# Performance work log

Hardware: AMD Instinct MI355X
Metric: run time of the kernel (lower is better)

## Reference

```python
import jax, jax.numpy as jnp
import numpy as np

D_MODEL = 1024
NUM_HEADS = 16
D_K = D_MODEL // NUM_HEADS


def setup_inputs() -> dict:
    key = jax.random.key(0)
    ks = jax.random.split(key, 11)
    B, S, D = 2, 2048, D_MODEL
    scale = 1.0 / np.sqrt(D)
    inp = {
        'queries': jax.random.normal(ks[0], (B, S, D), jnp.float32),
        'keys': jax.random.normal(ks[1], (B, S, D), jnp.float32),
        'values': jax.random.normal(ks[2], (B, S, D), jnp.float32),
        'w_q': jax.random.normal(ks[3], (D, D), jnp.float32) * scale,
        'b_q': jnp.zeros((D,), jnp.float32),
        'w_k': jax.random.normal(ks[4], (D, D), jnp.float32) * scale,
        'b_k': jnp.zeros((D,), jnp.float32),
        'w_v': jax.random.normal(ks[5], (D, D), jnp.float32) * scale,
        'b_v': jnp.zeros((D,), jnp.float32),
        'w_o': jax.random.normal(ks[6], (D, D), jnp.float32) * scale,
        'b_o': jnp.zeros((D,), jnp.float32),
    }
    return inp


def _split_heads(x):
    # [B, S, D] -> [B, H, S, d_k]
    B, S, _ = x.shape
    return x.reshape(B, S, NUM_HEADS, D_K).transpose(0, 2, 1, 3)


def reference(queries, keys, values, w_q, b_q, w_k, b_k, w_v, b_v, w_o, b_o):
    q = _split_heads(queries @ w_q.T + b_q)
    k = _split_heads(keys @ w_k.T + b_k)
    v = _split_heads(values @ w_v.T + b_v)
    # scaled dot-product attention: [B, H, Sq, Sk]
    scores = jnp.einsum('bhqd,bhkd->bhqk', q, k) / jnp.sqrt(jnp.asarray(D_K, q.dtype))
    weights = jax.nn.softmax(scores, axis=-1)
    attn = jnp.einsum('bhqk,bhkd->bhqd', weights, v)
    # merge heads: [B, Sq, D]
    B, H, S, dk = attn.shape
    merged = attn.transpose(0, 2, 1, 3).reshape(B, S, H * dk)
    return merged @ w_o.T + b_o
```

## Files before the change

kernel.cpp:

```cpp
#include <hip/hip_runtime.h>

typedef __attribute__((ext_vector_type(8))) short bf16x8;
typedef __attribute__((ext_vector_type(4))) short short4v;
typedef __attribute__((ext_vector_type(2))) unsigned int uint2v;
typedef __attribute__((ext_vector_type(4))) float f32x4;
typedef __attribute__((ext_vector_type(16))) float f32x16;
typedef __attribute__((ext_vector_type(4))) float float4v;
typedef unsigned short ushort_t;

__device__ __forceinline__ unsigned short f2bf(float x) {
    unsigned u = __float_as_uint(x);
    return (unsigned short)((u + 0x7fffu + ((u >> 16) & 1u)) >> 16);
}
__device__ __forceinline__ f32x4 mfma16(bf16x8 a, bf16x8 b, f32x4 c) {
    return __builtin_amdgcn_mfma_f32_16x16x32_bf16(a, b, c, 0, 0, 0);
}
__device__ __forceinline__ f32x16 mfma32(bf16x8 a, bf16x8 b, f32x16 c) {
    return __builtin_amdgcn_mfma_f32_32x32x16_bf16(a, b, c, 0, 0, 0);
}
__device__ __forceinline__ unsigned cvtpk(float lo, float hi) {
    unsigned r;
    asm("v_cvt_pk_bf16_f32 %0, %1, %2" : "=v"(r) : "v"(lo), "v"(hi));
    return r;
}
__device__ __forceinline__ bf16x8 pack4(unsigned w0, unsigned w1, unsigned w2, unsigned w3) {
    union { unsigned u[4]; bf16x8 v; } c;
    c.u[0] = w0; c.u[1] = w1; c.u[2] = w2; c.u[3] = w3;
    return c.v;
}

constexpr int GK = 1024;
constexpr int SLD = 72;
constexpr float QSCALE = 0.18033688011112042f;

__global__ __launch_bounds__(256)
void gemm_qkv2(const float* __restrict__ Aq, const float* __restrict__ Bq,
               const float* __restrict__ bq, ushort_t* __restrict__ Oq,
               const float* __restrict__ Ak, const float* __restrict__ Bk,
               const float* __restrict__ bk, ushort_t* __restrict__ Ok,
               const float* __restrict__ Avp, const float* __restrict__ Bv,
               const float* __restrict__ bv, ushort_t* __restrict__ Ov)
{
    __shared__ alignas(16) short Ah[128 * SLD];
    __shared__ alignas(16) short Bh[128 * SLD];

    const int bid = blockIdx.x;
    const int tid = threadIdx.x, lane = tid & 63, wv = tid >> 6;
    const int lr = lane & 15, lg = lane >> 4;
    const int r16 = tid >> 4, c4 = (tid & 15) * 4;

    if (bid < 512) {
        const int z = bid >> 8, fc = bid & 255;
        const float* A = z ? Ak : Aq;
        const float* B = z ? Bk : Bq;
        const float* bias = z ? bk : bq;
        ushort_t* O = z ? Ok : Oq;

        const int t = (fc & 7) * 32 + (fc >> 3);
        const int m0 = (t >> 3) * 128, n0 = (t & 7) * 128;
        const int wm = (wv >> 1) * 64, wn = (wv & 1) * 64;

        f32x4 acc[4][4] = {};
        float4v pfa[8], pfb[8];

        auto load_tiles = [&](int k0) {
            #pragma unroll
            for (int i = 0; i < 8; ++i) {
                pfa[i] = *(const float4v*)(A + (size_t)(m0 + r16 + 16 * i) * GK + k0 + c4);
                pfb[i] = *(const float4v*)(B + (size_t)(n0 + r16 + 16 * i) * GK + k0 + c4);
            }
        };
        auto store_tiles = [&]() {
            #pragma unroll
            for (int i = 0; i < 8; ++i) {
                uint2v wa, wb;
                wa.x = cvtpk(pfa[i][0], pfa[i][1]); wa.y = cvtpk(pfa[i][2], pfa[i][3]);
                wb.x = cvtpk(pfb[i][0], pfb[i][1]); wb.y = cvtpk(pfb[i][2], pfb[i][3]);
                *(uint2v*)(Ah + (r16 + 16 * i) * SLD + c4) = wa;
                *(uint2v*)(Bh + (r16 + 16 * i) * SLD + c4) = wb;
            }
        };

        load_tiles(0);
        for (int k0 = 0; k0 < GK; k0 += 64) {
            __syncthreads();
            store_tiles();
            __syncthreads();
            if (k0 + 64 < GK) load_tiles(k0 + 64);
            #pragma unroll
            for (int ks = 0; ks < 2; ++ks) {
                bf16x8 af[4], bfr[4];
                #pragma unroll
                for (int mi = 0; mi < 4; ++mi)
                    af[mi] = *(const bf16x8*)(Ah + (wm + mi * 16 + lr) * SLD + ks * 32 + lg * 8);
                #pragma unroll
                for (int ni = 0; ni < 4; ++ni)
                    bfr[ni] = *(const bf16x8*)(Bh + (wn + ni * 16 + lr) * SLD + ks * 32 + lg * 8);
                #pragma unroll
                for (int mi = 0; mi < 4; ++mi)
                    #pragma unroll
                    for (int ni = 0; ni < 4; ++ni)
                        acc[mi][ni] = mfma16(af[mi], bfr[ni], acc[mi][ni]);
            }
        }

        #pragma unroll
        for (int mi = 0; mi < 4; ++mi)
            #pragma unroll
            for (int ni = 0; ni < 4; ++ni) {
                const int gr = m0 + wm + mi * 16 + lg * 4;
                const int gc = n0 + wn + ni * 16 + lr;
                #pragma unroll
                for (int r = 0; r < 4; ++r) {
                    float val = acc[mi][ni][r] + bias[gc];
                    if (z == 0) val *= QSCALE;
                    O[(size_t)(gr + r) * 1024 + gc] = f2bf(val);
                }
            }
    } else {
        const int fc = bid - 512;
        const int t = (fc & 7) * 64 + (fc >> 3);
        const int nt = t >> 3, mt = t & 7;
        const int m0 = mt * 128, n0 = nt * 64;
        const int wm = (wv >> 1) * 64, wn = (wv & 1) * 32;

        f32x4 acc[4][2] = {};
        float4v pfa[8], pfb[4];

        auto load_tiles = [&](int k0) {
            #pragma unroll
            for (int i = 0; i < 8; ++i)
                pfa[i] = *(const float4v*)(Avp + (size_t)(m0 + r16 + 16 * i) * GK + k0 + c4);
            #pragma unroll
            for (int i = 0; i < 4; ++i)
                pfb[i] = *(const float4v*)(Bv + (size_t)(n0 + r16 + 16 * i) * GK + k0 + c4);
        };
        auto store_tiles = [&]() {
            #pragma unroll
            for (int i = 0; i < 8; ++i) {
                uint2v w;
                w.x = cvtpk(pfa[i][0], pfa[i][1]);
                w.y = cvtpk(pfa[i][2], pfa[i][3]);
                *(uint2v*)(Ah + (r16 + 16 * i) * SLD + c4) = w;
            }
            #pragma unroll
            for (int i = 0; i < 4; ++i) {
                uint2v w;
                w.x = cvtpk(pfb[i][0], pfb[i][1]);
                w.y = cvtpk(pfb[i][2], pfb[i][3]);
                *(uint2v*)(Bh + (r16 + 16 * i) * SLD + c4) = w;
            }
        };

        load_tiles(0);
        for (int k0 = 0; k0 < GK; k0 += 64) {
            __syncthreads();
            store_tiles();
            __syncthreads();
            if (k0 + 64 < GK) load_tiles(k0 + 64);
            #pragma unroll
            for (int ks = 0; ks < 2; ++ks) {
                bf16x8 af[4], bfr[2];
                #pragma unroll
                for (int mi = 0; mi < 4; ++mi)
                    af[mi] = *(const bf16x8*)(Ah + (wm + mi * 16 + lr) * SLD + ks * 32 + lg * 8);
                #pragma unroll
                for (int ni = 0; ni < 2; ++ni)
                    bfr[ni] = *(const bf16x8*)(Bh + (wn + ni * 16 + lr) * SLD + ks * 32 + lg * 8);
                #pragma unroll
                for (int mi = 0; mi < 4; ++mi)
                    #pragma unroll
                    for (int ni = 0; ni < 2; ++ni)
                        acc[mi][ni] = mfma16(af[mi], bfr[ni], acc[mi][ni]);
            }
        }

        #pragma unroll
        for (int mi = 0; mi < 4; ++mi)
            #pragma unroll
            for (int ni = 0; ni < 2; ++ni) {
                const int gr = m0 + wm + mi * 16 + lg * 4;
                const int gc = n0 + wn + ni * 16 + lr;
                #pragma unroll
                for (int r = 0; r < 4; ++r) {
                    float val = acc[mi][ni][r] + bv[gr + r];
                    Ov[(size_t)(gr + r) * 4096 + gc] = f2bf(val);
                }
            }
    }
}

__global__ __launch_bounds__(256)
void gemm_o(const ushort_t* __restrict__ A, const float* __restrict__ B,
            const float* __restrict__ bias, float* __restrict__ O)
{
    __shared__ alignas(16) short Ah[128 * SLD];
    __shared__ alignas(16) short Bh[64 * SLD];

    const int tid = threadIdx.x, lane = tid & 63, wv = tid >> 6;
    const int lr = lane & 15, lg = lane >> 4;

    const int f = blockIdx.x;
    const int t = (f & 7) * 64 + (f >> 3);
    const int mt = t >> 4, nt = t & 15;
    const int m0 = mt * 128, n0 = nt * 64;

    const int wm = (wv >> 1) * 64, wn = (wv & 1) * 32;
    const int r16 = tid >> 4, c4 = (tid & 15) * 4;
    const int r8 = tid >> 3, c8 = (tid & 7) * 8;

    f32x4 acc[4][2] = {};
    float4v pfb[4];
    bf16x8 pba[4];

    auto load_tiles = [&](int k0) {
        #pragma unroll
        for (int i = 0; i < 4; ++i)
            pba[i] = *(const bf16x8*)(A + (size_t)(m0 + r8 + 32 * i) * GK + k0 + c8);
        #pragma unroll
        for (int i = 0; i < 4; ++i)
            pfb[i] = *(const float4v*)(B + (size_t)(n0 + r16 + 16 * i) * GK + k0 + c4);
    };
    auto store_tiles = [&]() {
        #pragma unroll
        for (int i = 0; i < 4; ++i)
            *(bf16x8*)(Ah + (r8 + 32 * i) * SLD + c8) = pba[i];
        #pragma unroll
        for (int i = 0; i < 4; ++i) {
            uint2v w;
            w.x = cvtpk(pfb[i][0], pfb[i][1]);
            w.y = cvtpk(pfb[i][2], pfb[i][3]);
            *(uint2v*)(Bh + (r16 + 16 * i) * SLD + c4) = w;
        }
    };

    load_tiles(0);
    for (int k0 = 0; k0 < GK; k0 += 64) {
        __syncthreads();
        store_tiles();
        __syncthreads();
        if (k0 + 64 < GK) load_tiles(k0 + 64);
        #pragma unroll
        for (int ks = 0; ks < 2; ++ks) {
            bf16x8 af[4], bfr[2];
            #pragma unroll
            for (int mi = 0; mi < 4; ++mi)
                af[mi] = *(const bf16x8*)(Ah + (wm + mi * 16 + lr) * SLD + ks * 32 + lg * 8);
            #pragma unroll
            for (int ni = 0; ni < 2; ++ni)
                bfr[ni] = *(const bf16x8*)(Bh + (wn + ni * 16 + lr) * SLD + ks * 32 + lg * 8);
            #pragma unroll
            for (int mi = 0; mi < 4; ++mi)
                #pragma unroll
                for (int ni = 0; ni < 2; ++ni)
                    acc[mi][ni] = mfma16(af[mi], bfr[ni], acc[mi][ni]);
        }
    }

    #pragma unroll
    for (int mi = 0; mi < 4; ++mi)
        #pragma unroll
        for (int ni = 0; ni < 2; ++ni) {
            const int gr = m0 + wm + mi * 16 + lg * 4;
            const int gc = n0 + wn + ni * 16 + lr;
            #pragma unroll
            for (int r = 0; r < 4; ++r)
                O[(size_t)(gr + r) * 1024 + gc] = acc[mi][ni][r] + bias[gc];
        }
}

constexpr int SEQ = 2048, DM = 1024;

__device__ __forceinline__ bf16x8 lds_rd(const short* base, int row, int chunk) {
    return *(const bf16x8*)(base + row * 64 + ((chunk * 8) ^ ((row & 7) << 3)));
}

__global__ __launch_bounds__(512, 4)
void attn15_kernel(const ushort_t* __restrict__ Qb, const ushort_t* __restrict__ Kb,
                   const ushort_t* __restrict__ Vt,  ushort_t* __restrict__ Mrg)
{
    __shared__ alignas(16) float smem_f[8704];
    short* s16 = (short*)smem_f;

    const int tid = threadIdx.x, lane = tid & 63, wv = tid >> 6;
    const int l31 = lane & 31, lg2 = lane >> 5;
    const int qg = wv >> 1, khalf = wv & 1;

    const int f = blockIdx.y * 16 + blockIdx.x;
    const int g = (f & 7) * 64 + (f >> 3);
    const int qt = g & 15, bh = g >> 4;
    const int b = bh >> 4, h = bh & 15;
    const size_t seq0 = (size_t)b * SEQ;
    const int col0 = h * 64;

    const int qrow = qt * 128 + qg * 32 + l31;
    bf16x8 qh[4];
    #pragma unroll
    for (int kc = 0; kc < 4; ++kc)
        qh[kc] = *(const bf16x8*)(Qb + (seq0 + qrow) * DM + col0 + kc * 16 + lg2 * 8);

    f32x16 accT0 = {}, accT1 = {};
    float l_run = 0.f;

    const int sr = tid >> 3, sc8 = (tid & 7) * 8;
    const int wi = sr * 64 + (sc8 ^ ((sr & 7) << 3));
    const int kb = khalf * 32;
    const int cb = khalf * 4;

    bf16x8 gkh, gvv;
    auto load_regs = [&](int kt) {
        gkh = *(const bf16x8*)(Kb + (seq0 + kt + sr) * DM + col0 + sc8);
        gvv = *(const bf16x8*)(Vt + (size_t)(col0 + sr) * 4096 + seq0 + kt + sc8);
    };
    auto write_buf = [&](int buf) {
        *(bf16x8*)(s16 + buf * 8192 + wi) = gkh;
        *(bf16x8*)(s16 + buf * 8192 + 4096 + wi) = gvv;
    };

    load_regs(0);
    write_buf(0);

    for (int t = 0; t < 32; ++t) {
        __syncthreads();
        if (t < 31) load_regs((t + 1) * 64);
        const short* Ksh = s16 + (t & 1) * 8192;
        const short* Vsm = Ksh + 4096;

        f32x16 s0 = {};
        #pragma unroll
        for (int kc = 0; kc < 4; ++kc) {
            const int c = kc * 2 + lg2;
            bf16x8 kh0 = lds_rd(Ksh, kb + l31, c);
            s0 = mfma32(kh0, qh[kc], s0);
        }

        float rs = 0.f;
        #pragma unroll
        for (int i = 0; i < 16; ++i) {
            float p = __builtin_amdgcn_exp2f(s0[i]);
            s0[i] = p; rs += p;
        }
        l_run += rs;

        unsigned pk0[4][2];
        #pragma unroll
        for (int m = 0; m < 4; ++m) {
            pk0[m][0] = cvtpk(s0[4 * m],     s0[4 * m + 1]);
            pk0[m][1] = cvtpk(s0[4 * m + 2], s0[4 * m + 3]);
        }
        bf16x8 pa[2];
        #pragma unroll
        for (int u = 0; u < 2; ++u) {
            const unsigned pe0 = pk0[2 * u][0],     pe1 = pk0[2 * u][1];
            const unsigned po0 = pk0[2 * u + 1][0], po1 = pk0[2 * u + 1][1];
            const unsigned sd0 = lg2 ? pe0 : po0;
            const unsigned sd1 = lg2 ? pe1 : po1;
            const unsigned rc0 = (unsigned)__shfl_xor((int)sd0, 32);
            const unsigned rc1 = (unsigned)__shfl_xor((int)sd1, 32);
            const unsigned a0 = lg2 ? rc0 : pe0;
            const unsigned a1 = lg2 ? rc1 : pe1;
            const unsigned a2 = lg2 ? po0 : rc0;
            const unsigned a3 = lg2 ? po1 : rc1;
            pa[u] = pack4(a0, a1, a2, a3);
        }

        #pragma unroll
        for (int u = 0; u < 2; ++u) {
            const int c = cb + u * 2 + lg2;
            bf16x8 v0 = lds_rd(Vsm, l31,      c);
            bf16x8 v1 = lds_rd(Vsm, l31 + 32, c);
            accT0 = mfma32(v0, pa[u], accT0);
            accT1 = mfma32(v1, pa[u], accT1);
        }

        if (t < 31) write_buf((t + 1) & 1);
    }

    const float lfull = l_run + __shfl_xor(l_run, 32);
    float* slot = smem_f + (qg * 64 + lane) * 33;
    __syncthreads();
    if (khalf == 1) {
        slot[0] = lfull;
        #pragma unroll
        for (int i = 0; i < 16; ++i) { slot[1 + i] = accT0[i]; slot[17 + i] = accT1[i]; }
    }
    __syncthreads();
    if (khalf == 0) {
        const float inv = 1.0f / (lfull + slot[0]);
        #pragma unroll
        for (int reg = 0; reg < 16; ++reg) {
            const int d = (reg & 3) + 8 * (reg >> 2) + 4 * lg2;
            float o0 = (accT0[reg] + slot[1 + reg])  * inv;
            float o1 = (accT1[reg] + slot[17 + reg]) * inv;
            Mrg[(seq0 + qrow) * DM + col0 + d]      = f2bf(o0);
            Mrg[(seq0 + qrow) * DM + col0 + d + 32] = f2bf(o1);
        }
    }
}

extern "C" void kernel_launch(void* const* d_in, const int* in_sizes, int n_in,
                              void* d_out, int out_size, void* d_ws, size_t ws_size,
                              hipStream_t stream)
{
    const float* queries = (const float*)d_in[0];
    const float* keys    = (const float*)d_in[1];
    const float* values  = (const float*)d_in[2];
    const float* w_q = (const float*)d_in[3];
    const float* b_q = (const float*)d_in[4];
    const float* w_k = (const float*)d_in[5];
    const float* b_k = (const float*)d_in[6];
    const float* w_v = (const float*)d_in[7];
    const float* b_v = (const float*)d_in[8];
    const float* w_o = (const float*)d_in[9];
    const float* b_o = (const float*)d_in[10];

    const size_t MB = 1u << 20;
    char* ws = (char*)d_ws;
    ushort_t* Qb = (ushort_t*)(ws);
    ushort_t* Kb = (ushort_t*)(ws + 8 * MB);
    ushort_t* Mb = (ushort_t*)(ws + 16 * MB);
    ushort_t* Vt = (ushort_t*)d_out;

    dim3 blk(256);

    hipLaunchKernelGGL(gemm_qkv2, dim3(1024), blk, 0, stream,
                       queries, w_q, b_q, Qb,
                       keys,    w_k, b_k, Kb,
                       w_v,  values, b_v, Vt);
    hipLaunchKernelGGL(attn15_kernel, dim3(16, 32), dim3(512), 0, stream,
                       Qb, Kb, Vt, Mb);
    hipLaunchKernelGGL(gemm_o, dim3(512), blk, 0, stream,
                       Mb, w_o, b_o, (float*)d_out);
}
```

Baseline: 118.4 us.

## Double-buffer LDS tiles in GEMMs and raise wave priority around attention MFMAs

All three GEMM kernels (QKV projection, V projection branch, output projection) now use two shared-memory buffers. The next tile is stored into the alternate buffer after the MFMA loop, so each k-step needs one barrier instead of two and the fp32-to-bf16 conversion and LDS stores overlap with other waves' compute. The attention kernel is renamed and wraps its QK and PV MFMA sections in s_setprio(1)/s_setprio(0) to favour waves issuing matrix work. The cost is doubled LDS per GEMM block, which may lower occupancy.

```diff
diff --git a/kernel.cpp b/kernel.cpp
--- a/kernel.cpp
+++ b/kernel.cpp
@@ -41,8 +41,8 @@
                const float* __restrict__ Avp, const float* __restrict__ Bv,
                const float* __restrict__ bv, ushort_t* __restrict__ Ov)
 {
-    __shared__ alignas(16) short Ah[128 * SLD];
-    __shared__ alignas(16) short Bh[128 * SLD];
+    __shared__ alignas(16) short Ah[2][128 * SLD];
+    __shared__ alignas(16) short Bh[2][128 * SLD];
 
     const int bid = blockIdx.x;
     const int tid = threadIdx.x, lane = tid & 63, wv = tid >> 6;
@@ -56,8 +56,8 @@
         const float* bias = z ? bk : bq;
         ushort_t* O = z ? Ok : Oq;
 
-        const int t = (fc & 7) * 32 + (fc >> 3);
-        const int m0 = (t >> 3) * 128, n0 = (t & 7) * 128;
+        const int t0 = (fc & 7) * 32 + (fc >> 3);
+        const int m0 = (t0 >> 3) * 128, n0 = (t0 & 7) * 128;
         const int wm = (wv >> 1) * 64, wn = (wv & 1) * 64;
 
         f32x4 acc[4][4] = {};
@@ -70,38 +70,40 @@
                 pfb[i] = *(const float4v*)(B + (size_t)(n0 + r16 + 16 * i) * GK + k0 + c4);
             }
         };
-        auto store_tiles = [&]() {
+        auto store_tiles = [&](int buf) {
             #pragma unroll
             for (int i = 0; i < 8; ++i) {
                 uint2v wa, wb;
                 wa.x = cvtpk(pfa[i][0], pfa[i][1]); wa.y = cvtpk(pfa[i][2], pfa[i][3]);
                 wb.x = cvtpk(pfb[i][0], pfb[i][1]); wb.y = cvtpk(pfb[i][2], pfb[i][3]);
-                *(uint2v*)(Ah + (r16 + 16 * i) * SLD + c4) = wa;
-                *(uint2v*)(Bh + (r16 + 16 * i) * SLD + c4) = wb;
+                *(uint2v*)(&Ah[buf][(r16 + 16 * i) * SLD + c4]) = wa;
+                *(uint2v*)(&Bh[buf][(r16 + 16 * i) * SLD + c4]) = wb;
             }
         };
 
         load_tiles(0);
-        for (int k0 = 0; k0 < GK; k0 += 64) {
+        store_tiles(0);
+        for (int t = 0; t < 16; ++t) {
             __syncthreads();
-            store_tiles();
-            __syncthreads();
-            if (k0 + 64 < GK) load_tiles(k0 + 64);
+            if (t < 15) load_tiles((t + 1) * 64);
+            const short* As = Ah[t & 1];
+            const short* Bs = Bh[t & 1];
             #pragma unroll
             for (int ks = 0; ks < 2; ++ks) {
                 bf16x8 af[4], bfr[4];
                 #pragma unroll
                 for (int mi = 0; mi < 4; ++mi)
-                    af[mi] = *(const bf16x8*)(Ah + (wm + mi * 16 + lr) * SLD + ks * 32 + lg * 8);
+                    af[mi] = *(const bf16x8*)(As + (wm + mi * 16 + lr) * SLD + ks * 32 + lg * 8);
                 #pragma unroll
                 for (int ni = 0; ni < 4; ++ni)
-                    bfr[ni] = *(const bf16x8*)(Bh + (wn + ni * 16 + lr) * SLD + ks * 32 + lg * 8);
+                    bfr[ni] = *(const bf16x8*)(Bs + (wn + ni * 16 + lr) * SLD + ks * 32 + lg * 8);
                 #pragma unroll
                 for (int mi = 0; mi < 4; ++mi)
                     #pragma unroll
                     for (int ni = 0; ni < 4; ++ni)
                         acc[mi][ni] = mfma16(af[mi], bfr[ni], acc[mi][ni]);
             }
+            if (t < 15) store_tiles((t + 1) & 1);
         }
 
         #pragma unroll
@@ -119,8 +121,8 @@
             }
     } else {
         const int fc = bid - 512;
-        const int t = (fc & 7) * 64 + (fc >> 3);
-        const int nt = t >> 3, mt = t & 7;
+        const int t0 = (fc & 7) * 64 + (fc >> 3);
+        const int nt = t0 >> 3, mt = t0 & 7;
         const int m0 = mt * 128, n0 = nt * 64;
         const int wm = (wv >> 1) * 64, wn = (wv & 1) * 32;
 
@@ -135,44 +137,46 @@
             for (int i = 0; i < 4; ++i)
                 pfb[i] = *(const float4v*)(Bv + (size_t)(n0 + r16 + 16 * i) * GK + k0 + c4);
         };
-        auto store_tiles = [&]() {
+        auto store_tiles = [&](int buf) {
             #pragma unroll
             for (int i = 0; i < 8; ++i) {
                 uint2v w;
                 w.x = cvtpk(pfa[i][0], pfa[i][1]);
                 w.y = cvtpk(pfa[i][2], pfa[i][3]);
-                *(uint2v*)(Ah + (r16 + 16 * i) * SLD + c4) = w;
+                *(uint2v*)(&Ah[buf][(r16 + 16 * i) * SLD + c4]) = w;
             }
             #pragma unroll
             for (int i = 0; i < 4; ++i) {
                 uint2v w;
                 w.x = cvtpk(pfb[i][0], pfb[i][1]);
                 w.y = cvtpk(pfb[i][2], pfb[i][3]);
-                *(uint2v*)(Bh + (r16 + 16 * i) * SLD + c4) = w;
+                *(uint2v*)(&Bh[buf][(r16 + 16 * i) * SLD + c4]) = w;
             }
         };
 
         load_tiles(0);
-        for (int k0 = 0; k0 < GK; k0 += 64) {
+        store_tiles(0);
+        for (int t = 0; t < 16; ++t) {
             __syncthreads();
-            store_tiles();
-            __syncthreads();
-            if (k0 + 64 < GK) load_tiles(k0 + 64);
+            if (t < 15) load_tiles((t + 1) * 64);
+            const short* As = Ah[t & 1];
+            const short* Bs = Bh[t & 1];
             #pragma unroll
             for (int ks = 0; ks < 2; ++ks) {
                 bf16x8 af[4], bfr[2];
                 #pragma unroll
                 for (int mi = 0; mi < 4; ++mi)
-                    af[mi] = *(const bf16x8*)(Ah + (wm + mi * 16 + lr) * SLD + ks * 32 + lg * 8);
+                    af[mi] = *(const bf16x8*)(As + (wm + mi * 16 + lr) * SLD + ks * 32 + lg * 8);
                 #pragma unroll
                 for (int ni = 0; ni < 2; ++ni)
-                    bfr[ni] = *(const bf16x8*)(Bh + (wn + ni * 16 + lr) * SLD + ks * 32 + lg * 8);
+                    bfr[ni] = *(const bf16x8*)(Bs + (wn + ni * 16 + lr) * SLD + ks * 32 + lg * 8);
                 #pragma unroll
                 for (int mi = 0; mi < 4; ++mi)
                     #pragma unroll
                     for (int ni = 0; ni < 2; ++ni)
                         acc[mi][ni] = mfma16(af[mi], bfr[ni], acc[mi][ni]);
             }
+            if (t < 15) store_tiles((t + 1) & 1);
         }
 
         #pragma unroll
@@ -194,15 +198,15 @@
 void gemm_o(const ushort_t* __restrict__ A, const float* __restrict__ B,
             const float* __restrict__ bias, float* __restrict__ O)
 {
-    __shared__ alignas(16) short Ah[128 * SLD];
-    __shared__ alignas(16) short Bh[64 * SLD];
+    __shared__ alignas(16) short Ah[2][128 * SLD];
+    __shared__ alignas(16) short Bh[2][64 * SLD];
 
     const int tid = threadIdx.x, lane = tid & 63, wv = tid >> 6;
     const int lr = lane & 15, lg = lane >> 4;
 
     const int f = blockIdx.x;
-    const int t = (f & 7) * 64 + (f >> 3);
-    const int mt = t >> 4, nt = t & 15;
+    const int t0 = (f & 7) * 64 + (f >> 3);
+    const int mt = t0 >> 4, nt = t0 & 15;
     const int m0 = mt * 128, n0 = nt * 64;
 
     const int wm = (wv >> 1) * 64, wn = (wv & 1) * 32;
@@ -221,40 +225,42 @@
         for (int i = 0; i < 4; ++i)
             pfb[i] = *(const float4v*)(B + (size_t)(n0 + r16 + 16 * i) * GK + k0 + c4);
     };
-    auto store_tiles = [&]() {
+    auto store_tiles = [&](int buf) {
         #pragma unroll
         for (int i = 0; i < 4; ++i)
-            *(bf16x8*)(Ah + (r8 + 32 * i) * SLD + c8) = pba[i];
+            *(bf16x8*)(&Ah[buf][(r8 + 32 * i) * SLD + c8]) = pba[i];
         #pragma unroll
         for (int i = 0; i < 4; ++i) {
             uint2v w;
             w.x = cvtpk(pfb[i][0], pfb[i][1]);
             w.y = cvtpk(pfb[i][2], pfb[i][3]);
-            *(uint2v*)(Bh + (r16 + 16 * i) * SLD + c4) = w;
+            *(uint2v*)(&Bh[buf][(r16 + 16 * i) * SLD + c4]) = w;
         }
     };
 
     load_tiles(0);
-    for (int k0 = 0; k0 < GK; k0 += 64) {
+    store_tiles(0);
+    for (int t = 0; t < 16; ++t) {
         __syncthreads();
-        store_tiles();
-        __syncthreads();
-        if (k0 + 64 < GK) load_tiles(k0 + 64);
+        if (t < 15) load_tiles((t + 1) * 64);
+        const short* As = Ah[t & 1];
+        const short* Bs = Bh[t & 1];
         #pragma unroll
         for (int ks = 0; ks < 2; ++ks) {
             bf16x8 af[4], bfr[2];
             #pragma unroll
             for (int mi = 0; mi < 4; ++mi)
-                af[mi] = *(const bf16x8*)(Ah + (wm + mi * 16 + lr) * SLD + ks * 32 + lg * 8);
+                af[mi] = *(const bf16x8*)(As + (wm + mi * 16 + lr) * SLD + ks * 32 + lg * 8);
             #pragma unroll
             for (int ni = 0; ni < 2; ++ni)
-                bfr[ni] = *(const bf16x8*)(Bh + (wn + ni * 16 + lr) * SLD + ks * 32 + lg * 8);
+                bfr[ni] = *(const bf16x8*)(Bs + (wn + ni * 16 + lr) * SLD + ks * 32 + lg * 8);
             #pragma unroll
             for (int mi = 0; mi < 4; ++mi)
                 #pragma unroll
                 for (int ni = 0; ni < 2; ++ni)
                     acc[mi][ni] = mfma16(af[mi], bfr[ni], acc[mi][ni]);
         }
+        if (t < 15) store_tiles((t + 1) & 1);
     }
 
     #pragma unroll
@@ -276,7 +282,7 @@
 }
 
 __global__ __launch_bounds__(512, 4)
-void attn15_kernel(const ushort_t* __restrict__ Qb, const ushort_t* __restrict__ Kb,
+void attn16_kernel(const ushort_t* __restrict__ Qb, const ushort_t* __restrict__ Kb,
                    const ushort_t* __restrict__ Vt,  ushort_t* __restrict__ Mrg)
 {
     __shared__ alignas(16) float smem_f[8704];
@@ -327,12 +333,14 @@
         const short* Vsm = Ksh + 4096;
 
         f32x16 s0 = {};
+        __builtin_amdgcn_s_setprio(1);
         #pragma unroll
         for (int kc = 0; kc < 4; ++kc) {
             const int c = kc * 2 + lg2;
             bf16x8 kh0 = lds_rd(Ksh, kb + l31, c);
             s0 = mfma32(kh0, qh[kc], s0);
         }
+        __builtin_amdgcn_s_setprio(0);
 
         float rs = 0.f;
         #pragma unroll
@@ -364,6 +372,7 @@
             pa[u] = pack4(a0, a1, a2, a3);
         }
 
+        __builtin_amdgcn_s_setprio(1);
         #pragma unroll
         for (int u = 0; u < 2; ++u) {
             const int c = cb + u * 2 + lg2;
@@ -372,6 +381,7 @@
             accT0 = mfma32(v0, pa[u], accT0);
             accT1 = mfma32(v1, pa[u], accT1);
         }
+        __builtin_amdgcn_s_setprio(0);
 
         if (t < 31) write_buf((t + 1) & 1);
     }
@@ -427,7 +437,7 @@
                        queries, w_q, b_q, Qb,
                        keys,    w_k, b_k, Kb,
                        w_v,  values, b_v, Vt);
-    hipLaunchKernelGGL(attn15_kernel, dim3(16, 32), dim3(512), 0, stream,
+    hipLaunchKernelGGL(attn16_kernel, dim3(16, 32), dim3(512), 0, stream,
                        Qb, Kb, Vt, Mb);
     hipLaunchKernelGGL(gemm_o, dim3(512), blk, 0, stream,
                        Mb, w_o, b_o, (float*)d_out);
```

After: 123.9 us. 4.6% more time.
